# Performance work log

Hardware: AMD Instinct MI355X
Metric: run time of the kernel (lower is better)

The kernel has to match this reference:

```python
import jax, jax.numpy as jnp
import numpy as np

N = 100000   # nodes
E = 600000   # edges
B = 1000     # graphs
H = 128      # GCN hidden dim


def setup_inputs() -> dict:
    key = jax.random.key(0)
    ks = jax.random.split(key, 12)
    x = jax.random.normal(ks[0], (N, 1), jnp.float32)
    edge_index = jax.random.randint(ks[1], (2, E), 0, N)
    batch = (jnp.arange(N) // (N // B)).astype(jnp.int32)  # sorted, non-empty segments
    y = jax.random.normal(ks[2], (B,), jnp.float32)
    # GCNConv params (Glorot-ish scales)
    gcn_w = jax.random.normal(ks[3], (1, H), jnp.float32)
    gcn_b = jnp.zeros((H,), jnp.float32)
    # Linear(128, 64)
    w2 = jax.random.normal(ks[4], (H, 64), jnp.float32) / np.sqrt(H)
    b2 = jnp.zeros((64,), jnp.float32)
    # Linear(65, 32)
    w3 = jax.random.normal(ks[5], (65, 32), jnp.float32) / np.sqrt(65.0)
    b3 = jnp.zeros((32,), jnp.float32)
    # Linear(32, 1)
    w4 = jax.random.normal(ks[6], (32, 1), jnp.float32) / np.sqrt(32.0)
    b4 = jnp.zeros((1,), jnp.float32)
    return dict(x=x, y=y, edge_index=edge_index, batch=batch,
                gcn_w=gcn_w, gcn_b=gcn_b, w2=w2, b2=b2, w3=w3, b3=b3, w4=w4, b4=b4)


def reference(x, y, edge_index, batch, gcn_w, gcn_b, w2, b2, w3, b3, w4, b4):
    src, dst = edge_index[0], edge_index[1]
    # GCNConv: D^{-1/2} (A + I) D^{-1/2} X W + b, degrees include self-loops
    deg = jax.ops.segment_sum(jnp.ones((E,), x.dtype), dst, num_segments=N) + 1.0
    dinv = jax.lax.rsqrt(deg)                       # [N]
    h = x @ gcn_w                                   # [N, H]
    norm = dinv[src] * dinv[dst]                    # [E]
    msg = h[src] * norm[:, None]                    # [E, H] gather + scale
    agg = jax.ops.segment_sum(msg, dst, num_segments=N)
    agg = agg + h * (dinv * dinv)[:, None]          # self-loop contribution
    x1 = jax.nn.relu(agg + gcn_b)                   # [N, H]
    # global_mean_pool over batch ids
    sums = jax.ops.segment_sum(x1, batch, num_segments=B)        # [B, H]
    cnts = jax.ops.segment_sum(jnp.ones((N,), x.dtype), batch, num_segments=B)
    pooled = sums / cnts[:, None]                   # [B, H]
    cell = jax.nn.relu(pooled @ w2 + b2)            # [B, 64]
    concat = jnp.concatenate([cell, y[:, None]], axis=-1)  # [B, 65]
    hfc = jax.nn.relu(concat @ w3 + b3)             # dropout is identity at eval
    out = (hfc @ w4 + b4).reshape(-1)               # [B]
    return out
```

## Files before the change

kernel.cpp:

```cpp
#include <hip/hip_runtime.h>
#include <hip/hip_bf16.h>

__global__ void deg_kernel(const int* __restrict__ dst, float* __restrict__ deg, int E) {
    int e = blockIdx.x * blockDim.x + threadIdx.x;
    if (e < E) atomicAdd(&deg[dst[e]], 1.0f);
}

__global__ void edge_kernel(const int* __restrict__ src, const int* __restrict__ dst,
                            const float* __restrict__ x, const float* __restrict__ deg,
                            float* __restrict__ s, int E) {
    int e = blockIdx.x * blockDim.x + threadIdx.x;
    if (e < E) {
        int a = src[e];
        int b = dst[e];
        float u = x[a] * rsqrtf(deg[a] + 1.0f);
        atomicAdd(&s[b], u);
    }
}

__global__ void pool_mlp_kernel(const float* __restrict__ x, const float* __restrict__ y,
                                const float* __restrict__ deg, const float* __restrict__ s,
                                const float* __restrict__ gcn_w, const float* __restrict__ gcn_b,
                                const float* __restrict__ w2, const float* __restrict__ b2,
                                const float* __restrict__ w3, const float* __restrict__ b3,
                                const float* __restrict__ w4, const float* __restrict__ b4,
                                float* __restrict__ out, int npg) {
    const int b = blockIdx.x;
    const int tid = threadIdx.x;

    __shared__ float t_lds[128];
    __shared__ float pooled[128];
    __shared__ float concat[65];
    __shared__ float hfc[32];

    if (tid < npg) {
        int n = b * npg + tid;
        float dinv = rsqrtf(deg[n] + 1.0f);
        t_lds[tid] = dinv * (s[n] + x[n] * dinv);
    }
    __syncthreads();

    {
        float gw = gcn_w[tid];
        float gb = gcn_b[tid];
        float sum = 0.0f;
        for (int i = 0; i < npg; ++i)
            sum += fmaxf(t_lds[i] * gw + gb, 0.0f);
        pooled[tid] = sum * (1.0f / (float)npg);
    }
    __syncthreads();

    if (tid < 64) {
        float dot = b2[tid];
        for (int k = 0; k < 128; ++k)
            dot += pooled[k] * w2[k * 64 + tid];
        concat[tid] = fmaxf(dot, 0.0f);
    }
    if (tid == 64) concat[64] = y[b];
    __syncthreads();

    if (tid < 32) {
        float dot = b3[tid];
        for (int i = 0; i < 65; ++i)
            dot += concat[i] * w3[i * 32 + tid];
        hfc[tid] = fmaxf(dot, 0.0f);
    }
    __syncthreads();

    if (tid == 0) {
        float dot = b4[0];
        for (int j = 0; j < 32; ++j)
            dot += hfc[j] * w4[j];
        out[b] = dot;
    }
}

extern "C" void kernel_launch(void* const* d_in, const int* in_sizes, int n_in,
                              void* d_out, int out_size, void* d_ws, size_t ws_size,
                              hipStream_t stream) {
    const float* x     = (const float*)d_in[0];
    const float* y     = (const float*)d_in[1];
    const int*   ei    = (const int*)d_in[2];
    const float* gcn_w = (const float*)d_in[4];
    const float* gcn_b = (const float*)d_in[5];
    const float* w2    = (const float*)d_in[6];
    const float* b2    = (const float*)d_in[7];
    const float* w3    = (const float*)d_in[8];
    const float* b3    = (const float*)d_in[9];
    const float* w4    = (const float*)d_in[10];
    const float* b4    = (const float*)d_in[11];
    float* out = (float*)d_out;

    const int N = in_sizes[0];
    const int B = in_sizes[1];
    const int E = in_sizes[2] / 2;
    const int npg = N / B;

    const int* src = ei;
    const int* dst = ei + E;

    float* deg = (float*)d_ws;
    float* s   = deg + N;

    hipMemsetAsync(d_ws, 0, (size_t)2 * N * sizeof(float), stream);

    deg_kernel<<<(E + 255) / 256, 256, 0, stream>>>(dst, deg, E);
    edge_kernel<<<(E + 255) / 256, 256, 0, stream>>>(src, dst, x, deg, s, E);
    pool_mlp_kernel<<<B, 128, 0, stream>>>(x, y, deg, s, gcn_w, gcn_b,
                                           w2, b2, w3, b3, w4, b4, out, npg);
}
```

Before: 81.99 us.

## Fuse degree, edge scatter and pool-MLP into one persistent kernel with grid barriers

```diff
diff --git a/kernel.cpp b/kernel.cpp
--- a/kernel.cpp
+++ b/kernel.cpp
@@ -1,77 +1,127 @@
 #include <hip/hip_runtime.h>
 #include <hip/hip_bf16.h>
 
-__global__ void deg_kernel(const int* __restrict__ dst, float* __restrict__ deg, int E) {
-    int e = blockIdx.x * blockDim.x + threadIdx.x;
-    if (e < E) atomicAdd(&deg[dst[e]], 1.0f);
+#define NB 512
+#define NT 256
+
+__device__ __forceinline__ void gbar(unsigned* cnt) {
+    __syncthreads();
+    if (threadIdx.x == 0) {
+        __threadfence();
+        __hip_atomic_fetch_add(cnt, 1u, __ATOMIC_ACQ_REL, __HIP_MEMORY_SCOPE_AGENT);
+        while (__hip_atomic_load(cnt, __ATOMIC_ACQUIRE, __HIP_MEMORY_SCOPE_AGENT) < NB) {
+            __builtin_amdgcn_s_sleep(2);
+        }
+        __threadfence();
+    }
+    __syncthreads();
 }
 
-__global__ void edge_kernel(const int* __restrict__ src, const int* __restrict__ dst,
-                            const float* __restrict__ x, const float* __restrict__ deg,
-                            float* __restrict__ s, int E) {
-    int e = blockIdx.x * blockDim.x + threadIdx.x;
-    if (e < E) {
-        int a = src[e];
-        int b = dst[e];
-        float u = x[a] * rsqrtf(deg[a] + 1.0f);
-        atomicAdd(&s[b], u);
-    }
+__device__ __forceinline__ float aload(const float* p) {
+    return __hip_atomic_load(p, __ATOMIC_RELAXED, __HIP_MEMORY_SCOPE_AGENT);
 }
 
-__global__ void pool_mlp_kernel(const float* __restrict__ x, const float* __restrict__ y,
-                                const float* __restrict__ deg, const float* __restrict__ s,
-                                const float* __restrict__ gcn_w, const float* __restrict__ gcn_b,
-                                const float* __restrict__ w2, const float* __restrict__ b2,
-                                const float* __restrict__ w3, const float* __restrict__ b3,
-                                const float* __restrict__ w4, const float* __restrict__ b4,
-                                float* __restrict__ out, int npg) {
-    const int b = blockIdx.x;
+__global__ __launch_bounds__(NT, 4)
+void gnn_fused(const float* __restrict__ x, const float* __restrict__ y,
+               const int* __restrict__ src, const int* __restrict__ dst,
+               const float* __restrict__ gcn_w, const float* __restrict__ gcn_b,
+               const float* __restrict__ w2, const float* __restrict__ b2,
+               const float* __restrict__ w3, const float* __restrict__ b3,
+               const float* __restrict__ w4, const float* __restrict__ b4,
+               float* __restrict__ out,
+               float* __restrict__ deg, float* __restrict__ s,
+               unsigned* __restrict__ bar,
+               int N, int E, int B, int npg)
+{
+    const int g = blockIdx.x * NT + threadIdx.x;
+    const int G = NB * NT;
     const int tid = threadIdx.x;
+
+    for (int i = g; i < 2 * N; i += G)
+        __hip_atomic_store(&deg[i], 0.0f, __ATOMIC_RELAXED, __HIP_MEMORY_SCOPE_AGENT);
+    gbar(&bar[0]);
+
+    const int E4 = E >> 2;
+    const int4* dst4 = reinterpret_cast<const int4*>(dst);
+    for (int v = g; v < E4; v += G) {
+        int4 d = dst4[v];
+        atomicAdd(&deg[d.x], 1.0f);
+        atomicAdd(&deg[d.y], 1.0f);
+        atomicAdd(&deg[d.z], 1.0f);
+        atomicAdd(&deg[d.w], 1.0f);
+    }
+    for (int e = (E4 << 2) + g; e < E; e += G)
+        atomicAdd(&deg[dst[e]], 1.0f);
+    gbar(&bar[1]);
+
+    const int4* src4 = reinterpret_cast<const int4*>(src);
+    for (int v = g; v < E4; v += G) {
+        int4 a = src4[v];
+        int4 b = dst4[v];
+        float vx = x[a.x] * rsqrtf(aload(&deg[a.x]) + 1.0f);
+        float vy = x[a.y] * rsqrtf(aload(&deg[a.y]) + 1.0f);
+        float vz = x[a.z] * rsqrtf(aload(&deg[a.z]) + 1.0f);
+        float vw = x[a.w] * rsqrtf(aload(&deg[a.w]) + 1.0f);
+        atomicAdd(&s[b.x], vx);
+        atomicAdd(&s[b.y], vy);
+        atomicAdd(&s[b.z], vz);
+        atomicAdd(&s[b.w], vw);
+    }
+    for (int e = (E4 << 2) + g; e < E; e += G) {
+        int a = src[e];
+        atomicAdd(&s[dst[e]], x[a] * rsqrtf(aload(&deg[a]) + 1.0f));
+    }
+    gbar(&bar[2]);
 
     __shared__ float t_lds[128];
     __shared__ float pooled[128];
     __shared__ float concat[65];
     __shared__ float hfc[32];
 
-    if (tid < npg) {
-        int n = b * npg + tid;
-        float dinv = rsqrtf(deg[n] + 1.0f);
-        t_lds[tid] = dinv * (s[n] + x[n] * dinv);
-    }
-    __syncthreads();
+    for (int b = blockIdx.x; b < B; b += NB) {
+        if (tid < npg) {
+            int n = b * npg + tid;
+            float dv = aload(&deg[n]);
+            float sv = aload(&s[n]);
+            float di = rsqrtf(dv + 1.0f);
+            t_lds[tid] = di * sv + x[n] * di * di;
+        }
+        __syncthreads();
 
-    {
-        float gw = gcn_w[tid];
-        float gb = gcn_b[tid];
-        float sum = 0.0f;
-        for (int i = 0; i < npg; ++i)
-            sum += fmaxf(t_lds[i] * gw + gb, 0.0f);
-        pooled[tid] = sum * (1.0f / (float)npg);
-    }
-    __syncthreads();
+        if (tid < 128) {
+            float gw = gcn_w[tid];
+            float gb = gcn_b[tid];
+            float sum = 0.0f;
+            for (int i = 0; i < npg; ++i)
+                sum += fmaxf(t_lds[i] * gw + gb, 0.0f);
+            pooled[tid] = sum * (1.0f / (float)npg);
+        }
+        __syncthreads();
 
-    if (tid < 64) {
-        float dot = b2[tid];
-        for (int k = 0; k < 128; ++k)
-            dot += pooled[k] * w2[k * 64 + tid];
-        concat[tid] = fmaxf(dot, 0.0f);
-    }
-    if (tid == 64) concat[64] = y[b];
-    __syncthreads();
+        if (tid < 64) {
+            float dot = b2[tid];
+            for (int k = 0; k < 128; ++k)
+                dot += pooled[k] * w2[k * 64 + tid];
+            concat[tid] = fmaxf(dot, 0.0f);
+        }
+        if (tid == 64) concat[64] = y[b];
+        __syncthreads();
 
-    if (tid < 32) {
-        float dot = b3[tid];
-        for (int i = 0; i < 65; ++i)
-            dot += concat[i] * w3[i * 32 + tid];
-        hfc[tid] = fmaxf(dot, 0.0f);
-    }
-    __syncthreads();
+        if (tid < 32) {
+            float dot = b3[tid];
+            for (int i = 0; i < 65; ++i)
+                dot += concat[i] * w3[i * 32 + tid];
+            hfc[tid] = fmaxf(dot, 0.0f);
+        }
+        __syncthreads();
 
-    if (tid == 0) {
-        float dot = b4[0];
-        for (int j = 0; j < 32; ++j)
-            dot += hfc[j] * w4[j];
-        out[b] = dot;
+        if (tid == 0) {
+            float dot = b4[0];
+            for (int j = 0; j < 32; ++j)
+                dot += hfc[j] * w4[j];
+            out[b] = dot;
+        }
+        __syncthreads();
     }
 }
 
@@ -99,13 +149,13 @@
     const int* src = ei;
     const int* dst = ei + E;
 
-    float* deg = (float*)d_ws;
+    unsigned* bar = (unsigned*)d_ws;
+    float* deg = (float*)((char*)d_ws + 64);
     float* s   = deg + N;
 
-    hipMemsetAsync(d_ws, 0, (size_t)2 * N * sizeof(float), stream);
+    hipMemsetAsync(d_ws, 0, 64, stream);
 
-    deg_kernel<<<(E + 255) / 256, 256, 0, stream>>>(dst, deg, E);
-    edge_kernel<<<(E + 255) / 256, 256, 0, stream>>>(src, dst, x, deg, s, E);
-    pool_mlp_kernel<<<B, 128, 0, stream>>>(x, y, deg, s, gcn_w, gcn_b,
-                                           w2, b2, w3, b3, w4, b4, out, npg);
+    gnn_fused<<<dim3(NB), dim3(NT), 0, stream>>>(
+        x, y, src, dst, gcn_w, gcn_b, w2, b2, w3, b3, w4, b4,
+        out, deg, s, bar, N, E, B, npg);
 }
```

After: 278.0 us. 239% more time.

## Privatize degree and scatter accumulators per XCC with workgroup-scope atomics

Applied to the files above, without the earlier changes.

```diff
diff --git a/kernel.cpp b/kernel.cpp
--- a/kernel.cpp
+++ b/kernel.cpp
@@ -1,30 +1,85 @@
 #include <hip/hip_runtime.h>
 #include <hip/hip_bf16.h>
 
-__global__ void deg_kernel(const int* __restrict__ dst, float* __restrict__ deg, int E) {
-    int e = blockIdx.x * blockDim.x + threadIdx.x;
-    if (e < E) atomicAdd(&deg[dst[e]], 1.0f);
+#define NCOPY 8
+
+__device__ __forceinline__ unsigned xcc_id() {
+    unsigned x;
+    asm volatile("s_getreg_b32 %0, hwreg(HW_REG_XCC_ID)" : "=s"(x));
+    return x & (NCOPY - 1);
 }
 
-__global__ void edge_kernel(const int* __restrict__ src, const int* __restrict__ dst,
-                            const float* __restrict__ x, const float* __restrict__ deg,
-                            float* __restrict__ s, int E) {
-    int e = blockIdx.x * blockDim.x + threadIdx.x;
-    if (e < E) {
-        int a = src[e];
-        int b = dst[e];
-        float u = x[a] * rsqrtf(deg[a] + 1.0f);
-        atomicAdd(&s[b], u);
-    }
+__device__ __forceinline__ void atomic_add_l2(float* p, float v) {
+    __hip_atomic_fetch_add(p, v, __ATOMIC_RELAXED, __HIP_MEMORY_SCOPE_WORKGROUP);
 }
 
-__global__ void pool_mlp_kernel(const float* __restrict__ x, const float* __restrict__ y,
-                                const float* __restrict__ deg, const float* __restrict__ s,
+__global__ void zero_kernel(float4* __restrict__ p, int n4) {
+    int i = blockIdx.x * blockDim.x + threadIdx.x;
+    int G = gridDim.x * blockDim.x;
+    float4 z = make_float4(0.f, 0.f, 0.f, 0.f);
+    for (; i < n4; i += G) p[i] = z;
+}
+
+__global__ void deg_kernel(const int* __restrict__ dst, float* __restrict__ degc,
+                           int N, int E) {
+    float* my = degc + (size_t)xcc_id() * N;
+    int g = blockIdx.x * blockDim.x + threadIdx.x;
+    int G = gridDim.x * blockDim.x;
+    const int E4 = E >> 2;
+    const int4* dst4 = reinterpret_cast<const int4*>(dst);
+    for (int v = g; v < E4; v += G) {
+        int4 d = dst4[v];
+        atomic_add_l2(&my[d.x], 1.0f);
+        atomic_add_l2(&my[d.y], 1.0f);
+        atomic_add_l2(&my[d.z], 1.0f);
+        atomic_add_l2(&my[d.w], 1.0f);
+    }
+    for (int e = (E4 << 2) + g; e < E; e += G) atomic_add_l2(&my[dst[e]], 1.0f);
+}
+
+__global__ void reduce_deg_kernel(const float* __restrict__ x,
+                                  const float* __restrict__ degc,
+                                  float* __restrict__ di, float* __restrict__ u,
+                                  int N) {
+    int n = blockIdx.x * blockDim.x + threadIdx.x;
+    if (n >= N) return;
+    float d = 1.0f;
+    #pragma unroll
+    for (int i = 0; i < NCOPY; ++i) d += degc[(size_t)i * N + n];
+    float r = rsqrtf(d);
+    di[n] = r;
+    u[n]  = x[n] * r;
+}
+
+__global__ void scatter_kernel(const int* __restrict__ src, const int* __restrict__ dst,
+                               const float* __restrict__ u, float* __restrict__ sc,
+                               int N, int E) {
+    float* my = sc + (size_t)xcc_id() * N;
+    int g = blockIdx.x * blockDim.x + threadIdx.x;
+    int G = gridDim.x * blockDim.x;
+    const int E4 = E >> 2;
+    const int4* src4 = reinterpret_cast<const int4*>(src);
+    const int4* dst4 = reinterpret_cast<const int4*>(dst);
+    for (int v = g; v < E4; v += G) {
+        int4 a = src4[v];
+        int4 b = dst4[v];
+        float ux = u[a.x], uy = u[a.y], uz = u[a.z], uw = u[a.w];
+        atomic_add_l2(&my[b.x], ux);
+        atomic_add_l2(&my[b.y], uy);
+        atomic_add_l2(&my[b.z], uz);
+        atomic_add_l2(&my[b.w], uw);
+    }
+    for (int e = (E4 << 2) + g; e < E; e += G) atomic_add_l2(&my[dst[e]], u[src[e]]);
+}
+
+__global__ void pool_mlp_kernel(const float* __restrict__ y,
+                                const float* __restrict__ di, const float* __restrict__ u,
+                                const float* __restrict__ sc,
                                 const float* __restrict__ gcn_w, const float* __restrict__ gcn_b,
                                 const float* __restrict__ w2, const float* __restrict__ b2,
                                 const float* __restrict__ w3, const float* __restrict__ b3,
                                 const float* __restrict__ w4, const float* __restrict__ b4,
-                                float* __restrict__ out, int npg) {
+                                float* __restrict__ out, int npg, int N) {
     const int b = blockIdx.x;
     const int tid = threadIdx.x;
 
@@ -35,8 +90,10 @@
 
     if (tid < npg) {
         int n = b * npg + tid;
-        float dinv = rsqrtf(deg[n] + 1.0f);
-        t_lds[tid] = dinv * (s[n] + x[n] * dinv);
+        float ssum = u[n];
+        #pragma unroll
+        for (int i = 0; i < NCOPY; ++i) ssum += sc[(size_t)i * N + n];
+        t_lds[tid] = di[n] * ssum;
     }
     __syncthreads();
 
@@ -99,13 +156,19 @@
     const int* src = ei;
     const int* dst = ei + E;
 
-    float* deg = (float*)d_ws;
-    float* s   = deg + N;
+    float* degc = (float*)d_ws;
+    float* sc   = degc + (size_t)NCOPY * N;
+    float* di   = sc   + (size_t)NCOPY * N;
+    float* u    = di + N;
 
-    hipMemsetAsync(d_ws, 0, (size_t)2 * N * sizeof(float), stream);
+    const int n4 = (2 * NCOPY * N) / 4;
+    zero_kernel<<<1024, 256, 0, stream>>>((float4*)degc, n4);
 
-    deg_kernel<<<(E + 255) / 256, 256, 0, stream>>>(dst, deg, E);
-    edge_kernel<<<(E + 255) / 256, 256, 0, stream>>>(src, dst, x, deg, s, E);
-    pool_mlp_kernel<<<B, 128, 0, stream>>>(x, y, deg, s, gcn_w, gcn_b,
-                                           w2, b2, w3, b3, w4, b4, out, npg);
+    const int E4 = E >> 2;
+    const int nblk = (E4 + 255) / 256;
+    deg_kernel<<<nblk, 256, 0, stream>>>(dst, degc, N, E);
+    reduce_deg_kernel<<<(N + 255) / 256, 256, 0, stream>>>(x, degc, di, u, N);
+    scatter_kernel<<<nblk, 256, 0, stream>>>(src, dst, u, sc, N, E);
+    pool_mlp_kernel<<<B, 128, 0, stream>>>(y, di, u, sc, gcn_w, gcn_b,
+                                           w2, b2, w3, b3, w4, b4, out, npg, N);
 }
```

Measured after the change: 82.46 us. About the same (+0.6%).
